# Optimization experiments

Measured on AMD Instinct MI355X. Metric: run time of the kernel, lower is better.

Reference implementation:

```python
import jax, jax.numpy as jnp
import numpy as np

B, CIN, COUT, H, W, K, PAD = 8, 64, 64, 128, 128, 3, 1
KK = K * K


def setup_inputs() -> dict:
    key = jax.random.key(0)
    k1, k2, k3, k4 = jax.random.split(key, 4)
    x = jax.random.normal(k1, (B, CIN, H, W), jnp.float32)
    # offset/mask conv: 3*K*K output channels (2*KK offsets + KK mask logits).
    # Original zero-inits these; we use small random weights so the irregular
    # gather path is actually exercised (zero offsets degenerate to plain conv).
    w_off = jax.random.normal(k2, (3 * KK, CIN, K, K), jnp.float32) * 0.01
    b_off = jax.random.normal(k3, (3 * KK,), jnp.float32) * 0.01
    w_dcn = jax.random.normal(k4, (COUT, CIN, K, K), jnp.float32) * (1.0 / np.sqrt(CIN * KK))
    return {"x": x, "w_off": w_off, "b_off": b_off, "w_dcn": w_dcn}


def _bilinear_gather(x, py, px):
    # x: [B,C,H,W]; py/px: [B,KK,H,W] float sample coordinates.
    # Zero padding: integer corners outside the image contribute 0 (torchvision semantics).
    Bn, C, Hn, Wn = x.shape
    y0 = jnp.floor(py).astype(jnp.int32)
    x0 = jnp.floor(px).astype(jnp.int32)
    y1, x1 = y0 + 1, x0 + 1
    wy1 = py - y0.astype(py.dtype)
    wy0 = 1.0 - wy1
    wx1 = px - x0.astype(px.dtype)
    wx0 = 1.0 - wx1
    xf = x.reshape(Bn, C, Hn * Wn)

    def g(iy, ix):
        valid = ((iy >= 0) & (iy < Hn) & (ix >= 0) & (ix < Wn)).astype(x.dtype)
        idx = (jnp.clip(iy, 0, Hn - 1) * Wn + jnp.clip(ix, 0, Wn - 1)).reshape(Bn, -1)
        v = jax.vmap(lambda xr, i: xr[:, i])(xf, idx).reshape(Bn, C, *iy.shape[1:])
        return v * valid[:, None]  # [B,C,KK,H,W]

    return ((wy0 * wx0)[:, None] * g(y0, x0) + (wy0 * wx1)[:, None] * g(y0, x1)
            + (wy1 * wx0)[:, None] * g(y1, x0) + (wy1 * wx1)[:, None] * g(y1, x1))


def reference(x, w_off, b_off, w_dcn):
    dn = ('NCHW', 'OIHW', 'NCHW')
    off = jax.lax.conv_general_dilated(x, w_off, (1, 1), [(PAD, PAD), (PAD, PAD)],
                                       dimension_numbers=dn) + b_off[None, :, None, None]
    o1, o2, m = off[:, :KK], off[:, KK:2 * KK], off[:, 2 * KK:]
    mask = jax.nn.sigmoid(m)                    # [B,KK,H,W]
    offset = jnp.concatenate([o1, o2], axis=1)  # [B,2KK,H,W], torch cat((o1,o2),dim=1)
    # torchvision interprets channel 2k as dy, 2k+1 as dx for kernel point k
    dy, dx = offset[:, 0::2], offset[:, 1::2]   # each [B,KK,H,W]
    ki = (jnp.arange(KK) // K - PAD).astype(x.dtype)
    kj = (jnp.arange(KK) % K - PAD).astype(x.dtype)
    py = jnp.arange(H, dtype=x.dtype)[None, None, :, None] + ki[None, :, None, None] + dy
    px = jnp.arange(W, dtype=x.dtype)[None, None, None, :] + kj[None, :, None, None] + dx
    val = _bilinear_gather(x, py, px) * mask[:, None]  # [B,C,KK,H,W]
    return jnp.einsum('bckhw,ock->bohw', val, w_dcn.reshape(COUT, CIN, KK))
```

## Files before the change

### kernel.cpp

```cpp
#include <hip/hip_runtime.h>

#define Bn 8
#define CINn 64
#define COUTn 64
#define Hn 128
#define Wn 128
#define KKn 9

typedef __attribute__((ext_vector_type(8))) short short8v;
typedef __attribute__((ext_vector_type(4))) float f32x4;

__device__ __forceinline__ unsigned short f2bf(float f) {
    unsigned u = __float_as_uint(f);
    unsigned r = (u + 0x7FFFu + ((u >> 16) & 1u)) >> 16;
    return (unsigned short)r;
}
__device__ __forceinline__ float bf2f(unsigned short u) {
    return __uint_as_float(((unsigned)u) << 16);
}

__launch_bounds__(256)
__global__ void xt_prep(const float* __restrict__ x, unsigned short* __restrict__ xt) {
    __shared__ unsigned short tile[128 * 68];
    const int blk = blockIdx.x;
    const int b = blk >> 7, y = blk & 127;
    const int t = threadIdx.x;
    const float* xb = x + (((long)b * CINn) << 14) + (y << 7);
#pragma unroll
    for (int i = 0; i < 32; ++i) {
        int e = i * 256 + t;
        int c = e >> 7, xx = e & 127;
        tile[xx * 68 + c] = f2bf(xb[((long)c << 14) + xx]);
    }
    __syncthreads();
    unsigned short* dst = xt + ((long)(b * 128 + y) << 13);
#pragma unroll
    for (int i = 0; i < 4; ++i) {
        int q = i * 256 + t;
        int xx = q >> 3, j = q & 7;
        const unsigned long long* src = (const unsigned long long*)&tile[xx * 68 + j * 8];
        unsigned long long v0 = src[0], v1 = src[1];
        unsigned long long* d = (unsigned long long*)&dst[q * 8];
        d[0] = v0; d[1] = v1;
    }
}

__global__ void wdcn_prep(const float* __restrict__ w_dcn, unsigned short* __restrict__ w2) {
    int i = blockIdx.x * 256 + threadIdx.x;
    if (i >= COUTn * CINn * KKn) return;
    int c = i & 63;
    int o = (i >> 6) & 63;
    int k = i >> 12;
    w2[i] = f2bf(w_dcn[(o * CINn + c) * KKn + k]);
}

__global__ void woffprep(const float* __restrict__ w_off, unsigned short* __restrict__ wofft) {
    int i = blockIdx.x * 256 + threadIdx.x;
    if (i >= 9 * 32 * 64) return;
    int c   = i & 63;
    int ch  = (i >> 6) & 31;
    int tap = i >> 11;
    wofft[i] = (ch < 27) ? f2bf(w_off[(ch * 64 + c) * 9 + tap]) : (unsigned short)0;
}

__launch_bounds__(256)
__global__ void offconv_direct(const unsigned short* __restrict__ xt,
                               const unsigned short* __restrict__ wofft,
                               const float* __restrict__ b_off,
                               unsigned short* __restrict__ offo) {
    int blk = blockIdx.x;
    blk = (blk & 7) * 64 + (blk >> 3);
    const int b  = blk >> 6, hp = blk & 63;
    const int r0 = hp * 2;
    const int t  = threadIdx.x;
    const int lane = t & 63, wv = t >> 6;
    const int r16 = lane & 15, sub = lane >> 4;
    const unsigned short* xtb = xt + ((long)b << 20);

    f32x4 acc[2][4];
#pragma unroll
    for (int mt = 0; mt < 2; ++mt)
#pragma unroll
        for (int nt = 0; nt < 4; ++nt) acc[mt][nt] = (f32x4){0.f, 0.f, 0.f, 0.f};

    const short8v zf = {0, 0, 0, 0, 0, 0, 0, 0};

#pragma unroll
    for (int di = 0; di < 3; ++di) {
#pragma unroll
        for (int dj = 0; dj < 3; ++dj) {
            const int tap = di * 3 + dj;
#pragma unroll
            for (int kk = 0; kk < 2; ++kk) {
                const int cc8 = (kk * 4 + sub) << 3;
                short8v a0 = *(const short8v*)(wofft + ((tap * 32 +      r16) << 6) + cc8);
                short8v a1 = *(const short8v*)(wofft + ((tap * 32 + 16 + r16) << 6) + cc8);
                short8v bfr[4];
#pragma unroll
                for (int nt = 0; nt < 4; ++nt) {
                    int ntile = wv * 4 + nt;
                    int y = r0 + (ntile >> 3) + di - 1;
                    int w = (ntile & 7) * 16 + r16 + dj - 1;
                    bool valid = (y >= 0 && y < Hn && w >= 0 && w < Wn);
                    int yc = valid ? y : 0, wc = valid ? w : 0;
                    short8v v = *(const short8v*)(xtb + (yc << 13) + (wc << 6) + cc8);
                    bfr[nt] = valid ? v : zf;
                }
#pragma unroll
                for (int nt = 0; nt < 4; ++nt) {
                    acc[0][nt] = __builtin_amdgcn_mfma_f32_16x16x32_bf16(a0, bfr[nt], acc[0][nt], 0, 0, 0);
                    acc[1][nt] = __builtin_amdgcn_mfma_f32_16x16x32_bf16(a1, bfr[nt], acc[1][nt], 0, 0, 0);
                }
            }
        }
    }

#pragma unroll
    for (int mt = 0; mt < 2; ++mt)
#pragma unroll
        for (int nt = 0; nt < 4; ++nt) {
            int ntile = wv * 4 + nt;
            int h = r0 + (ntile >> 3), w = (ntile & 7) * 16 + r16;
#pragma unroll
            for (int r = 0; r < 4; ++r) {
                int ch = mt * 16 + sub * 4 + r;
                if (ch < 27)
                    offo[(((long)(b * 27 + ch)) << 14) + (h << 7) + w] = f2bf(acc[mt][nt][r] + b_off[ch]);
            }
        }
}

__launch_bounds__(256)
__global__ void dcn_direct(const unsigned short* __restrict__ xt,
                           const unsigned short* __restrict__ offo,
                           const unsigned short* __restrict__ w2,
                           float* __restrict__ out) {
    int blk = blockIdx.x;
    blk = (blk & 7) * 128 + (blk >> 3);
    const int b = blk >> 7, h = blk & 127;
    const int t = threadIdx.x;
    const int lane = t & 63, wv = t >> 6;
    const int ohalf = wv & 1, phalf = wv >> 1;
    const int r16 = lane & 15, sub = lane >> 4;
    const unsigned short* xtb = xt + ((long)b << 20);
    const unsigned short* ob  = offo + (((long)b * 27) << 14) + (h << 7);

    f32x4 acc[2][4];
#pragma unroll
    for (int ot = 0; ot < 2; ++ot)
#pragma unroll
        for (int pt = 0; pt < 4; ++pt)
            acc[ot][pt] = (f32x4){0.f, 0.f, 0.f, 0.f};

    for (int k = 0; k < KKn; ++k) {
        const int ky = k / 3 - 1, kx = k % 3 - 1;
        int o00[4], o01[4], o10[4], o11[4];
        float q00[4], q01[4], q10[4], q11[4];
#pragma unroll
        for (int pt = 0; pt < 4; ++pt) {
            int pos = phalf * 64 + pt * 16 + r16;
            float dy = bf2f(ob[((long)(2 * k) << 14) + pos]);
            float dx = bf2f(ob[((long)(2 * k + 1) << 14) + pos]);
            float m  = bf2f(ob[((long)(18 + k) << 14) + pos]);
            m = 1.f / (1.f + __expf(-m));
            float py = (float)(h + ky) + dy;
            float px = (float)(pos + kx) + dx;
            float fy = floorf(py), fx = floorf(px);
            int y0 = (int)fy, x0 = (int)fx;
            float wy1 = py - fy, wx1 = px - fx;
            float a0 = (y0 >= 0     && y0 < Hn)     ? (1.f - wy1) * m : 0.f;
            float a1 = (y0 + 1 >= 0 && y0 + 1 < Hn) ? wy1 * m         : 0.f;
            float b0 = (x0 >= 0     && x0 < Wn)     ? (1.f - wx1)     : 0.f;
            float b1 = (x0 + 1 >= 0 && x0 + 1 < Wn) ? wx1             : 0.f;
            q00[pt] = a0 * b0; q01[pt] = a0 * b1; q10[pt] = a1 * b0; q11[pt] = a1 * b1;
            int y0c = min(max(y0, 0), Hn - 1), y1c = min(max(y0 + 1, 0), Hn - 1);
            int x0c = min(max(x0, 0), Wn - 1), x1c = min(max(x0 + 1, 0), Wn - 1);
            o00[pt] = (y0c << 13) + (x0c << 6); o01[pt] = (y0c << 13) + (x1c << 6);
            o10[pt] = (y1c << 13) + (x0c << 6); o11[pt] = (y1c << 13) + (x1c << 6);
        }

#pragma unroll
        for (int kk = 0; kk < 2; ++kk) {
            const int cc8 = (kk * 4 + sub) << 3;
            short8v af[2];
            af[0] = *(const short8v*)(w2 + (k << 12) + ((ohalf * 32 +      r16) << 6) + cc8);
            af[1] = *(const short8v*)(w2 + (k << 12) + ((ohalf * 32 + 16 + r16) << 6) + cc8);
            short8v bfr[4];
#pragma unroll
            for (int pt = 0; pt < 4; ++pt) {
                short8v c00 = *(const short8v*)(xtb + o00[pt] + cc8);
                short8v c01 = *(const short8v*)(xtb + o01[pt] + cc8);
                short8v c10 = *(const short8v*)(xtb + o10[pt] + cc8);
                short8v c11 = *(const short8v*)(xtb + o11[pt] + cc8);
                const unsigned* u00 = (const unsigned*)&c00;
                const unsigned* u01 = (const unsigned*)&c01;
                const unsigned* u10 = (const unsigned*)&c10;
                const unsigned* u11 = (const unsigned*)&c11;
                short8v bf;
                unsigned* ub = (unsigned*)&bf;
#pragma unroll
                for (int jj = 0; jj < 4; ++jj) {
                    float f00l = __uint_as_float(u00[jj] << 16), f00h = __uint_as_float(u00[jj] & 0xffff0000u);
                    float f01l = __uint_as_float(u01[jj] << 16), f01h = __uint_as_float(u01[jj] & 0xffff0000u);
                    float f10l = __uint_as_float(u10[jj] << 16), f10h = __uint_as_float(u10[jj] & 0xffff0000u);
                    float f11l = __uint_as_float(u11[jj] << 16), f11h = __uint_as_float(u11[jj] & 0xffff0000u);
                    float tl = q00[pt] * f00l + q01[pt] * f01l + q10[pt] * f10l + q11[pt] * f11l;
                    float th = q00[pt] * f00h + q01[pt] * f01h + q10[pt] * f10h + q11[pt] * f11h;
                    ub[jj] = (unsigned)f2bf(tl) | ((unsigned)f2bf(th) << 16);
                }
                bfr[pt] = bf;
            }
#pragma unroll
            for (int ot = 0; ot < 2; ++ot)
#pragma unroll
                for (int pt = 0; pt < 4; ++pt)
                    acc[ot][pt] = __builtin_amdgcn_mfma_f32_16x16x32_bf16(af[ot], bfr[pt], acc[ot][pt], 0, 0, 0);
        }
    }

    const long obase = (((long)b * COUTn) << 14) + (h << 7);
#pragma unroll
    for (int ot = 0; ot < 2; ++ot)
#pragma unroll
        for (int pt = 0; pt < 4; ++pt) {
#pragma unroll
            for (int r = 0; r < 4; ++r) {
                int o   = ohalf * 32 + ot * 16 + sub * 4 + r;
                int pos = phalf * 64 + pt * 16 + r16;
                out[obase + ((long)o << 14) + pos] = acc[ot][pt][r];
            }
        }
}

extern "C" void kernel_launch(void* const* d_in, const int* in_sizes, int n_in,
                              void* d_out, int out_size, void* d_ws, size_t ws_size,
                              hipStream_t stream) {
    const float* x     = (const float*)d_in[0];
    const float* w_off = (const float*)d_in[1];
    const float* b_off = (const float*)d_in[2];
    const float* w_dcn = (const float*)d_in[3];
    float* out = (float*)d_out;

    unsigned short* xt    = (unsigned short*)d_ws;
    unsigned short* w2    = (unsigned short*)((char*)d_ws + 16777216);
    unsigned short* wofft = (unsigned short*)((char*)d_ws + 16850944);
    unsigned short* offo  = (unsigned short*)((char*)d_ws + 16887808);

    xt_prep<<<Bn * Hn, 256, 0, stream>>>(x, xt);
    wdcn_prep<<<144, 256, 0, stream>>>(w_dcn, w2);
    woffprep<<<72, 256, 0, stream>>>(w_off, wofft);
    offconv_direct<<<512, 256, 0, stream>>>(xt, wofft, b_off, offo);
    dcn_direct<<<Bn * Hn, 256, 0, stream>>>(xt, offo, w2, out);
}
```

Measured before the change: 257.3 us.

## Retile offset conv to one row per block and DCN waves to all output channels

The offset conv now has each block handle a single output row instead of two, which doubles the grid to 1024 blocks and halves the accumulators per wave. In the DCN kernel each wave now covers all 64 output channels for 32 pixels, instead of 32 channels for 64 pixels. This halves the bilinear gather and interpolation work per wave, since each sampled pixel's gather is no longer duplicated across two waves, at the cost of loading four weight fragments instead of two. The trade is less redundant irregular gather and ALU work against more weight loads and a different register footprint.

```diff
diff --git a/kernel.cpp b/kernel.cpp
--- a/kernel.cpp
+++ b/kernel.cpp
@@ -69,24 +69,25 @@
                                const float* __restrict__ b_off,
                                unsigned short* __restrict__ offo) {
     int blk = blockIdx.x;
-    blk = (blk & 7) * 64 + (blk >> 3);
-    const int b  = blk >> 6, hp = blk & 63;
-    const int r0 = hp * 2;
-    const int t  = threadIdx.x;
+    blk = (blk & 7) * 128 + (blk >> 3);
+    const int b = blk >> 7, h = blk & 127;
+    const int t = threadIdx.x;
     const int lane = t & 63, wv = t >> 6;
     const int r16 = lane & 15, sub = lane >> 4;
     const unsigned short* xtb = xt + ((long)b << 20);
 
-    f32x4 acc[2][4];
+    f32x4 acc[2][2];
 #pragma unroll
     for (int mt = 0; mt < 2; ++mt)
 #pragma unroll
-        for (int nt = 0; nt < 4; ++nt) acc[mt][nt] = (f32x4){0.f, 0.f, 0.f, 0.f};
+        for (int ntl = 0; ntl < 2; ++ntl) acc[mt][ntl] = (f32x4){0.f, 0.f, 0.f, 0.f};
 
     const short8v zf = {0, 0, 0, 0, 0, 0, 0, 0};
 
 #pragma unroll
     for (int di = 0; di < 3; ++di) {
+        const int y = h + di - 1;
+        const bool yok = (y >= 0 && y < Hn);
 #pragma unroll
         for (int dj = 0; dj < 3; ++dj) {
             const int tap = di * 3 + dj;
@@ -95,21 +96,20 @@
                 const int cc8 = (kk * 4 + sub) << 3;
                 short8v a0 = *(const short8v*)(wofft + ((tap * 32 +      r16) << 6) + cc8);
                 short8v a1 = *(const short8v*)(wofft + ((tap * 32 + 16 + r16) << 6) + cc8);
-                short8v bfr[4];
-#pragma unroll
-                for (int nt = 0; nt < 4; ++nt) {
-                    int ntile = wv * 4 + nt;
-                    int y = r0 + (ntile >> 3) + di - 1;
-                    int w = (ntile & 7) * 16 + r16 + dj - 1;
-                    bool valid = (y >= 0 && y < Hn && w >= 0 && w < Wn);
-                    int yc = valid ? y : 0, wc = valid ? w : 0;
+                short8v bfr[2];
+#pragma unroll
+                for (int ntl = 0; ntl < 2; ++ntl) {
+                    int w = wv * 32 + ntl * 16 + r16 + dj - 1;
+                    bool valid = yok && (w >= 0 && w < Wn);
+                    int wc = valid ? w : 0;
+                    int yc = yok ? y : 0;
                     short8v v = *(const short8v*)(xtb + (yc << 13) + (wc << 6) + cc8);
-                    bfr[nt] = valid ? v : zf;
+                    bfr[ntl] = valid ? v : zf;
                 }
 #pragma unroll
-                for (int nt = 0; nt < 4; ++nt) {
-                    acc[0][nt] = __builtin_amdgcn_mfma_f32_16x16x32_bf16(a0, bfr[nt], acc[0][nt], 0, 0, 0);
-                    acc[1][nt] = __builtin_amdgcn_mfma_f32_16x16x32_bf16(a1, bfr[nt], acc[1][nt], 0, 0, 0);
+                for (int ntl = 0; ntl < 2; ++ntl) {
+                    acc[0][ntl] = __builtin_amdgcn_mfma_f32_16x16x32_bf16(a0, bfr[ntl], acc[0][ntl], 0, 0, 0);
+                    acc[1][ntl] = __builtin_amdgcn_mfma_f32_16x16x32_bf16(a1, bfr[ntl], acc[1][ntl], 0, 0, 0);
                 }
             }
         }
@@ -118,14 +118,13 @@
 #pragma unroll
     for (int mt = 0; mt < 2; ++mt)
 #pragma unroll
-        for (int nt = 0; nt < 4; ++nt) {
-            int ntile = wv * 4 + nt;
-            int h = r0 + (ntile >> 3), w = (ntile & 7) * 16 + r16;
+        for (int ntl = 0; ntl < 2; ++ntl) {
+            int w = wv * 32 + ntl * 16 + r16;
 #pragma unroll
             for (int r = 0; r < 4; ++r) {
                 int ch = mt * 16 + sub * 4 + r;
                 if (ch < 27)
-                    offo[(((long)(b * 27 + ch)) << 14) + (h << 7) + w] = f2bf(acc[mt][nt][r] + b_off[ch]);
+                    offo[(((long)(b * 27 + ch)) << 14) + (h << 7) + w] = f2bf(acc[mt][ntl][r] + b_off[ch]);
             }
         }
 }
@@ -140,25 +139,24 @@
     const int b = blk >> 7, h = blk & 127;
     const int t = threadIdx.x;
     const int lane = t & 63, wv = t >> 6;
-    const int ohalf = wv & 1, phalf = wv >> 1;
     const int r16 = lane & 15, sub = lane >> 4;
     const unsigned short* xtb = xt + ((long)b << 20);
     const unsigned short* ob  = offo + (((long)b * 27) << 14) + (h << 7);
 
-    f32x4 acc[2][4];
-#pragma unroll
-    for (int ot = 0; ot < 2; ++ot)
-#pragma unroll
-        for (int pt = 0; pt < 4; ++pt)
-            acc[ot][pt] = (f32x4){0.f, 0.f, 0.f, 0.f};
+    f32x4 acc[4][2];
+#pragma unroll
+    for (int ot = 0; ot < 4; ++ot)
+#pragma unroll
+        for (int ptl = 0; ptl < 2; ++ptl)
+            acc[ot][ptl] = (f32x4){0.f, 0.f, 0.f, 0.f};
 
     for (int k = 0; k < KKn; ++k) {
         const int ky = k / 3 - 1, kx = k % 3 - 1;
-        int o00[4], o01[4], o10[4], o11[4];
-        float q00[4], q01[4], q10[4], q11[4];
-#pragma unroll
-        for (int pt = 0; pt < 4; ++pt) {
-            int pos = phalf * 64 + pt * 16 + r16;
+        int o00[2], o01[2], o10[2], o11[2];
+        float q00[2], q01[2], q10[2], q11[2];
+#pragma unroll
+        for (int ptl = 0; ptl < 2; ++ptl) {
+            int pos = wv * 32 + ptl * 16 + r16;
             float dy = bf2f(ob[((long)(2 * k) << 14) + pos]);
             float dx = bf2f(ob[((long)(2 * k + 1) << 14) + pos]);
             float m  = bf2f(ob[((long)(18 + k) << 14) + pos]);
@@ -172,26 +170,27 @@
             float a1 = (y0 + 1 >= 0 && y0 + 1 < Hn) ? wy1 * m         : 0.f;
             float b0 = (x0 >= 0     && x0 < Wn)     ? (1.f - wx1)     : 0.f;
             float b1 = (x0 + 1 >= 0 && x0 + 1 < Wn) ? wx1             : 0.f;
-            q00[pt] = a0 * b0; q01[pt] = a0 * b1; q10[pt] = a1 * b0; q11[pt] = a1 * b1;
+            q00[ptl] = a0 * b0; q01[ptl] = a0 * b1; q10[ptl] = a1 * b0; q11[ptl] = a1 * b1;
             int y0c = min(max(y0, 0), Hn - 1), y1c = min(max(y0 + 1, 0), Hn - 1);
             int x0c = min(max(x0, 0), Wn - 1), x1c = min(max(x0 + 1, 0), Wn - 1);
-            o00[pt] = (y0c << 13) + (x0c << 6); o01[pt] = (y0c << 13) + (x1c << 6);
-            o10[pt] = (y1c << 13) + (x0c << 6); o11[pt] = (y1c << 13) + (x1c << 6);
+            o00[ptl] = (y0c << 13) + (x0c << 6); o01[ptl] = (y0c << 13) + (x1c << 6);
+            o10[ptl] = (y1c << 13) + (x0c << 6); o11[ptl] = (y1c << 13) + (x1c << 6);
         }
 
 #pragma unroll
         for (int kk = 0; kk < 2; ++kk) {
             const int cc8 = (kk * 4 + sub) << 3;
-            short8v af[2];
-            af[0] = *(const short8v*)(w2 + (k << 12) + ((ohalf * 32 +      r16) << 6) + cc8);
-            af[1] = *(const short8v*)(w2 + (k << 12) + ((ohalf * 32 + 16 + r16) << 6) + cc8);
-            short8v bfr[4];
-#pragma unroll
-            for (int pt = 0; pt < 4; ++pt) {
-                short8v c00 = *(const short8v*)(xtb + o00[pt] + cc8);
-                short8v c01 = *(const short8v*)(xtb + o01[pt] + cc8);
-                short8v c10 = *(const short8v*)(xtb + o10[pt] + cc8);
-                short8v c11 = *(const short8v*)(xtb + o11[pt] + cc8);
+            short8v af[4];
+#pragma unroll
+            for (int ot = 0; ot < 4; ++ot)
+                af[ot] = *(const short8v*)(w2 + (k << 12) + ((ot * 16 + r16) << 6) + cc8);
+            short8v bfr[2];
+#pragma unroll
+            for (int ptl = 0; ptl < 2; ++ptl) {
+                short8v c00 = *(const short8v*)(xtb + o00[ptl] + cc8);
+                short8v c01 = *(const short8v*)(xtb + o01[ptl] + cc8);
+                short8v c10 = *(const short8v*)(xtb + o10[ptl] + cc8);
+                short8v c11 = *(const short8v*)(xtb + o11[ptl] + cc8);
                 const unsigned* u00 = (const unsigned*)&c00;
                 const unsigned* u01 = (const unsigned*)&c01;
                 const unsigned* u10 = (const unsigned*)&c10;
@@ -204,30 +203,30 @@
                     float f01l = __uint_as_float(u01[jj] << 16), f01h = __uint_as_float(u01[jj] & 0xffff0000u);
                     float f10l = __uint_as_float(u10[jj] << 16), f10h = __uint_as_float(u10[jj] & 0xffff0000u);
                     float f11l = __uint_as_float(u11[jj] << 16), f11h = __uint_as_float(u11[jj] & 0xffff0000u);
-                    float tl = q00[pt] * f00l + q01[pt] * f01l + q10[pt] * f10l + q11[pt] * f11l;
-                    float th = q00[pt] * f00h + q01[pt] * f01h + q10[pt] * f10h + q11[pt] * f11h;
+                    float tl = q00[ptl] * f00l + q01[ptl] * f01l + q10[ptl] * f10l + q11[ptl] * f11l;
+                    float th = q00[ptl] * f00h + q01[ptl] * f01h + q10[ptl] * f10h + q11[ptl] * f11h;
                     ub[jj] = (unsigned)f2bf(tl) | ((unsigned)f2bf(th) << 16);
                 }
-                bfr[pt] = bf;
-            }
-#pragma unroll
-            for (int ot = 0; ot < 2; ++ot)
-#pragma unroll
-                for (int pt = 0; pt < 4; ++pt)
-                    acc[ot][pt] = __builtin_amdgcn_mfma_f32_16x16x32_bf16(af[ot], bfr[pt], acc[ot][pt], 0, 0, 0);
+                bfr[ptl] = bf;
+            }
+#pragma unroll
+            for (int ot = 0; ot < 4; ++ot)
+#pragma unroll
+                for (int ptl = 0; ptl < 2; ++ptl)
+                    acc[ot][ptl] = __builtin_amdgcn_mfma_f32_16x16x32_bf16(af[ot], bfr[ptl], acc[ot][ptl], 0, 0, 0);
         }
     }
 
     const long obase = (((long)b * COUTn) << 14) + (h << 7);
 #pragma unroll
-    for (int ot = 0; ot < 2; ++ot)
-#pragma unroll
-        for (int pt = 0; pt < 4; ++pt) {
+    for (int ot = 0; ot < 4; ++ot)
+#pragma unroll
+        for (int ptl = 0; ptl < 2; ++ptl) {
 #pragma unroll
             for (int r = 0; r < 4; ++r) {
-                int o   = ohalf * 32 + ot * 16 + sub * 4 + r;
-                int pos = phalf * 64 + pt * 16 + r16;
-                out[obase + ((long)o << 14) + pos] = acc[ot][pt][r];
+                int o   = ot * 16 + sub * 4 + r;
+                int pos = wv * 32 + ptl * 16 + r16;
+                out[obase + ((long)o << 14) + pos] = acc[ot][ptl][r];
             }
         }
 }
@@ -249,6 +248,6 @@
     xt_prep<<<Bn * Hn, 256, 0, stream>>>(x, xt);
     wdcn_prep<<<144, 256, 0, stream>>>(w_dcn, w2);
     woffprep<<<72, 256, 0, stream>>>(w_off, wofft);
-    offconv_direct<<<512, 256, 0, stream>>>(xt, wofft, b_off, offo);
+    offconv_direct<<<Bn * Hn, 256, 0, stream>>>(xt, wofft, b_off, offo);
     dcn_direct<<<Bn * Hn, 256, 0, stream>>>(xt, offo, w2, out);
 }
```

Result: faster. 242.4 us (-5.8%).
